# Optimization experiments

Hardware: AMD Instinct MI355X
Metric: run time of the kernel (lower is better)

## Reference

```python
import jax, jax.numpy as jnp
import numpy as np

N = 40000   # nodes
E = 600000  # edges
G = 64      # graphs
DIN = 128   # input feature dim
H = 128     # hidden_channels
L = 3       # num_layers


def setup_inputs() -> dict:
    key = jax.random.key(0)
    ks = jax.random.split(key, 16)
    s = 0.05
    inp = {}
    inp["x"] = jax.random.normal(ks[0], (N, DIN), jnp.float32)
    inp["edge_attr"] = jax.random.normal(ks[1], (E,), jnp.float32)
    inp["node_w"] = jax.random.normal(ks[2], (DIN, H), jnp.float32) * s
    inp["node_b"] = jnp.zeros((H,), jnp.float32)
    inp["edge_w"] = jax.random.normal(ks[3], (1, H), jnp.float32) * s
    inp["edge_b"] = jnp.zeros((H,), jnp.float32)
    inp["t"] = jnp.ones((L,), jnp.float32)  # learn_t init 1.0
    inp["lin1_w"] = jax.random.normal(ks[4], (L, H, 2 * H), jnp.float32) * s
    inp["lin1_b"] = jnp.zeros((L, 2 * H), jnp.float32)
    inp["ln1_g"] = jnp.ones((L, 2 * H), jnp.float32)
    inp["ln1_bt"] = jnp.zeros((L, 2 * H), jnp.float32)
    inp["lin2_w"] = jax.random.normal(ks[5], (L, 2 * H, H), jnp.float32) * s
    inp["lin2_b"] = jnp.zeros((L, H), jnp.float32)
    inp["blk_g"] = jnp.ones((L, H), jnp.float32)
    inp["blk_b"] = jnp.zeros((L, H), jnp.float32)
    inp["hw1"] = jax.random.normal(ks[6], (H, H // 2), jnp.float32) * s
    inp["hb1"] = jnp.zeros((H // 2,), jnp.float32)
    inp["hw2"] = jax.random.normal(ks[7], (H // 2, H // 4), jnp.float32) * s
    inp["hb2"] = jnp.zeros((H // 4,), jnp.float32)
    inp["hw3"] = jax.random.normal(ks[8], (H // 4, 1), jnp.float32) * s
    inp["hb3"] = jnp.zeros((1,), jnp.float32)
    inp["edge_index"] = jax.random.randint(ks[9], (2, E), 0, N, jnp.int32)
    inp["batch"] = jnp.sort(jax.random.randint(ks[10], (N,), 0, G, jnp.int32))
    return inp


def _layer_norm(v, g, b):
    mu = jnp.mean(v, axis=-1, keepdims=True)
    var = jnp.var(v, axis=-1, keepdims=True)
    return (v - mu) * jax.lax.rsqrt(var + 1e-5) * g + b


def reference(x, edge_attr, node_w, node_b, edge_w, edge_b, t,
              lin1_w, lin1_b, ln1_g, ln1_bt, lin2_w, lin2_b,
              blk_g, blk_b, hw1, hb1, hw2, hb2, hw3, hb3,
              edge_index, batch):
    src, dst = edge_index[0], edge_index[1]
    h = x @ node_w + node_b                       # [N, H]
    ea = edge_attr[:, None] @ edge_w + edge_b     # [E, H]

    def genconv(xn, i):
        # message: relu(x_j + e) + eps
        msg = jax.nn.relu(xn[src] + ea) + 1e-7    # [E, H]
        # scatter-softmax over dst with learnable temperature t
        logit = msg * t[i]
        m = jax.ops.segment_max(logit, dst, num_segments=N)
        m = jnp.where(jnp.isfinite(m), m, 0.0)    # isolated nodes
        ex = jnp.exp(logit - m[dst])
        den = jax.ops.segment_sum(ex, dst, num_segments=N)
        agg = jax.ops.segment_sum(ex * msg, dst, num_segments=N) / jnp.maximum(den, 1e-16)
        o = agg + xn                              # add root
        # GENConv MLP: Linear(H,2H) -> LayerNorm -> ReLU -> Linear(2H,H)
        o = jax.nn.relu(_layer_norm(o @ lin1_w[i] + lin1_b[i], ln1_g[i], ln1_bt[i]))
        return o @ lin2_w[i] + lin2_b[i]

    # layer 0: bare conv (as in the torch forward)
    h = genconv(h, 0)
    # layers 1..L-1: DeepGCNLayer res+ (norm -> act -> [dropout=id in eval] -> conv -> residual)
    for i in range(1, L):
        r = jax.nn.relu(_layer_norm(h, blk_g[i], blk_b[i]))
        h = h + genconv(r, i)
    # final norm+act uses layer 0's norm/act
    h = jax.nn.relu(_layer_norm(h, blk_g[0], blk_b[0]))
    # global mean pool over graphs
    cnt = jax.ops.segment_sum(jnp.ones((N,), h.dtype), batch, num_segments=G)
    pooled = jax.ops.segment_sum(h, batch, num_segments=G) / jnp.maximum(cnt, 1.0)[:, None]
    # MLP head (dropout = identity in eval)
    o = jax.nn.relu(pooled @ hw1 + hb1)
    o = jax.nn.relu(o @ hw2 + hb2)
    return o @ hw3 + hb3                          # [G, 1]
```

## Files before the change

### kernel.cpp

```cpp
#include <hip/hip_runtime.h>
#include <math.h>

#define NN 40000
#define NE 600000
#define NG 64
#define DIM_IN 128
#define HH 128
#define HH2 256

using half8 = __attribute__((ext_vector_type(8))) _Float16;
using half4 = __attribute__((ext_vector_type(4))) _Float16;
using h2    = __attribute__((ext_vector_type(2))) _Float16;
using f4    = __attribute__((ext_vector_type(4))) float;

__device__ __forceinline__ int lower_bound_dev(const int* a, int n, int key) {
    int lo = 0, hi = n;
    while (lo < hi) { int mid = (lo + hi) >> 1; if (a[mid] < key) lo = mid + 1; else hi = mid; }
    return lo;
}

#define NX (NN*DIM_IN)
#define NX4 (NX/4)
__global__ void convert_kernel(const float* __restrict__ x, const float* __restrict__ node_w,
                               const float* __restrict__ lin1_w, const float* __restrict__ lin2_w,
                               _Float16* __restrict__ xh, _Float16* __restrict__ nwt,
                               _Float16* __restrict__ w1t, _Float16* __restrict__ w2t)
{
    int id = blockIdx.x * blockDim.x + threadIdx.x;
    if (id < NX4) {
        float4 v = *(const float4*)(x + (size_t)id * 4);
        half4 o; o.x = (_Float16)v.x; o.y = (_Float16)v.y; o.z = (_Float16)v.z; o.w = (_Float16)v.w;
        *(half4*)(xh + (size_t)id * 4) = o;
        return;
    }
    id -= NX4;
    if (id < 16384) { int n = id >> 7, k = id & 127; nwt[id] = (_Float16)node_w[k*128 + n]; return; }
    id -= 16384;
    if (id < 98304) {
        int l = id >> 15, r = id & 32767;
        int n = r >> 7, k = r & 127;
        w1t[id] = (_Float16)lin1_w[l*32768 + k*256 + n];
        return;
    }
    id -= 98304;
    if (id < 98304) {
        int l = id >> 15, r = id & 32767;
        int n = r >> 8, k = r & 255;
        w2t[id] = (_Float16)lin2_w[l*32768 + k*128 + n];
    }
}

__global__ void count_rank_kernel(const int* __restrict__ dst, int* __restrict__ counts,
                                  int* __restrict__ rank) {
    int e = blockIdx.x * blockDim.x + threadIdx.x;
    if (e < NE) rank[e] = atomicAdd(&counts[dst[e]], 1);
}

__global__ __launch_bounds__(1024) void scanA_kernel(const int* __restrict__ counts,
                                                     int* __restrict__ tmp, int* __restrict__ btot) {
    __shared__ int wpre[16];
    int t = threadIdx.x, lane = t & 63, wid = t >> 6;
    int i = blockIdx.x * 1024 + t;
    int v = (i < NN) ? counts[i] : 0;
    int s = v;
    #pragma unroll
    for (int off = 1; off < 64; off <<= 1) {
        int u = __shfl_up(s, off, 64);
        if (lane >= off) s += u;
    }
    if (lane == 63) wpre[wid] = s;
    __syncthreads();
    if (t == 0) {
        int run = 0;
        #pragma unroll
        for (int j = 0; j < 16; ++j) { int xv = wpre[j]; wpre[j] = run; run += xv; }
        btot[blockIdx.x] = run;
    }
    __syncthreads();
    if (i < NN) tmp[i] = s + wpre[wid];
}

__global__ __launch_bounds__(64) void scanB_kernel(const int* __restrict__ btot,
                                                   int* __restrict__ boff, int nb) {
    int t = threadIdx.x;
    int v = (t < nb) ? btot[t] : 0;
    int s = v;
    #pragma unroll
    for (int off = 1; off < 64; off <<= 1) {
        int u = __shfl_up(s, off, 64);
        if (t >= off) s += u;
    }
    if (t < nb) boff[t] = s - v;
}

__global__ __launch_bounds__(1024) void scanC_kernel(const int* __restrict__ tmp,
                                                     const int* __restrict__ boff,
                                                     int* __restrict__ rowp) {
    int i = blockIdx.x * 1024 + threadIdx.x;
    if (i < NN) rowp[i + 1] = tmp[i] + boff[blockIdx.x];
    if (i == 0) rowp[0] = 0;
}

__global__ void fill2_kernel(const int* __restrict__ src, const int* __restrict__ dst,
                             const float* __restrict__ eattr, const int* __restrict__ rowp,
                             const int* __restrict__ rank, int2* __restrict__ rec) {
    int e = blockIdx.x * blockDim.x + threadIdx.x;
    if (e < NE) {
        int pos = rowp[dst[e]] + rank[e];
        rec[pos] = make_int2(src[e], __float_as_int(eattr[e]));
    }
}

__global__ __launch_bounds__(256) void agg_kernel(
    const _Float16* __restrict__ xh,
    const int* __restrict__ row_ptr,
    const int2* __restrict__ rec,
    const float* __restrict__ ew, const float* __restrict__ eb,
    const float* __restrict__ tptr, int layer,
    _Float16* __restrict__ oh)
{
    int d = blockIdx.x * 4 + (threadIdx.x >> 6);
    int lane = threadIdx.x & 63;
    int c0 = 2 * lane;
    float tc = tptr[layer];
    float ew0 = ew[c0], eb0 = eb[c0];
    float ew1 = ew[c0 + 1], eb1 = eb[c0 + 1];
    int beg = row_ptr[d], end = row_ptr[d + 1];
    float den0 = 0.f, num0 = 0.f, den1 = 0.f, num1 = 0.f;
    for (int base = beg; base < end; base += 64) {
        int cnt = min(64, end - base);
        int2 mv = rec[base + min(lane, cnt - 1)];
        int sv = mv.x;
        float av = __int_as_float(mv.y);
        h2 gA[8], gB[8]; float aA[8], aB[8];
        auto issue = [&](h2 (&g)[8], float (&aa)[8], int j0) {
            #pragma unroll
            for (int u = 0; u < 8; ++u) {
                int jj = min(j0 + u, cnt - 1);
                int s = __shfl(sv, jj, 64);
                aa[u] = __shfl(av, jj, 64);
                g[u] = *(const h2*)(xh + ((size_t)s << 7) + c0);
            }
        };
        auto consume = [&](h2 (&g)[8], float (&aa)[8], int j0) {
            int lim = min(8, cnt - j0);
            #pragma unroll
            for (int u = 0; u < 8; ++u) {
                if (u < lim) {
                    float m0 = fmaxf(__fmaf_rn(aa[u], ew0, eb0) + (float)g[u].x, 0.f) + 1e-7f;
                    float m1 = fmaxf(__fmaf_rn(aa[u], ew1, eb1) + (float)g[u].y, 0.f) + 1e-7f;
                    float e0 = __expf(m0 * tc), e1 = __expf(m1 * tc);
                    den0 += e0; num0 = __fmaf_rn(e0, m0, num0);
                    den1 += e1; num1 = __fmaf_rn(e1, m1, num1);
                }
            }
        };
        issue(gA, aA, 0);
        for (int j0 = 0; j0 < cnt; j0 += 16) {
            if (j0 + 8 < cnt)  issue(gB, aB, j0 + 8);
            consume(gA, aA, j0);
            if (j0 + 16 < cnt) issue(gA, aA, j0 + 16);
            if (j0 + 8 < cnt)  consume(gB, aB, j0 + 8);
        }
    }
    h2 sv2 = *(const h2*)(xh + ((size_t)d << 7) + c0);
    float o0 = num0 / fmaxf(den0, 1e-16f) + (float)sv2.x;
    float o1 = num1 / fmaxf(den1, 1e-16f) + (float)sv2.y;
    h2 ov; ov.x = (_Float16)o0; ov.y = (_Float16)o1;
    *(h2*)(oh + ((size_t)d << 7) + c0) = ov;
}

__global__ __launch_bounds__(256) void gemm_mfma(
    const _Float16* __restrict__ A, const _Float16* __restrict__ Bt,
    const float* __restrict__ bias, _Float16* __restrict__ C,
    int M, int N, int K)
{
    constexpr int LDA = 40;
    __shared__ _Float16 As[64 * LDA];
    __shared__ _Float16 Bs[128 * LDA];
    int t = threadIdx.x;
    int row0 = blockIdx.y * 64;
    int col0 = blockIdx.x * 128;
    int w = t >> 6, lane = t & 63;
    int wm = w & 1, wn = w >> 1;
    int q = lane >> 4, l16 = lane & 15;
    f4 acc[2][4];
    #pragma unroll
    for (int i = 0; i < 2; ++i)
        #pragma unroll
        for (int j = 0; j < 4; ++j)
            acc[i][j] = (f4){0.f, 0.f, 0.f, 0.f};

    for (int k0 = 0; k0 < K; k0 += 32) {
        {
            int r = t >> 2, seg = t & 3;
            *(float4*)&As[r * LDA + seg * 8] =
                *(const float4*)(A + (size_t)(row0 + r) * K + k0 + seg * 8);
        }
        #pragma unroll
        for (int i = 0; i < 2; ++i) {
            int idx = t + i * 256;
            int r = idx >> 2, seg = idx & 3;
            *(float4*)&Bs[r * LDA + seg * 8] =
                *(const float4*)(Bt + (size_t)(col0 + r) * K + k0 + seg * 8);
        }
        __syncthreads();
        half8 af[2], bf[4];
        #pragma unroll
        for (int i = 0; i < 2; ++i)
            af[i] = *(const half8*)&As[(wm * 32 + i * 16 + l16) * LDA + q * 8];
        #pragma unroll
        for (int j = 0; j < 4; ++j)
            bf[j] = *(const half8*)&Bs[(wn * 64 + j * 16 + l16) * LDA + q * 8];
        #pragma unroll
        for (int i = 0; i < 2; ++i)
            #pragma unroll
            for (int j = 0; j < 4; ++j)
                acc[i][j] = __builtin_amdgcn_mfma_f32_16x16x32_f16(af[i], bf[j], acc[i][j], 0, 0, 0);
        __syncthreads();
    }
    #pragma unroll
    for (int j = 0; j < 4; ++j) {
        int col = col0 + wn * 64 + j * 16 + l16;
        float bv = bias[col];
        #pragma unroll
        for (int i = 0; i < 2; ++i) {
            int rbase = row0 + wm * 32 + i * 16 + q * 4;
            #pragma unroll
            for (int rg = 0; rg < 4; ++rg)
                C[(size_t)(rbase + rg) * N + col] = (_Float16)(acc[i][j][rg] + bv);
        }
    }
}

template<int RES>
__global__ __launch_bounds__(256) void mlp_fused(
    const _Float16* __restrict__ Ain,
    const _Float16* __restrict__ w1t,
    const float* __restrict__ b1,
    const float* __restrict__ g1, const float* __restrict__ bt1,
    const _Float16* __restrict__ w2t,
    const float* __restrict__ b2,
    float* __restrict__ h,
    const float* __restrict__ bg, const float* __restrict__ bb,
    _Float16* __restrict__ xout)
{
    constexpr int LDA = 136;
    constexpr int LDB = 40;
    constexpr int LDM = 264;
    __shared__ _Float16 As[64 * LDA];
    __shared__ _Float16 Bs[256 * LDB];
    __shared__ _Float16 midh[64 * LDM];
    __shared__ float ssum[64][2], ssum2[64][2];
    int t = threadIdx.x;
    int row0 = blockIdx.x * 64;
    int w = t >> 6, lane = t & 63;
    int wm = w & 1, wn = w >> 1;
    int q = lane >> 4, l16 = lane & 15;

    #pragma unroll
    for (int p = 0; p < 4; ++p) {
        int idx = t + p * 256;
        int r = idx >> 4, seg = idx & 15;
        *(float4*)&As[r * LDA + seg * 8] =
            *(const float4*)(Ain + (size_t)(row0 + r) * 128 + seg * 8);
    }

    f4 acc[2][8];
    #pragma unroll
    for (int i = 0; i < 2; ++i)
        #pragma unroll
        for (int j = 0; j < 8; ++j)
            acc[i][j] = (f4){0.f, 0.f, 0.f, 0.f};
    for (int k0 = 0; k0 < 128; k0 += 32) {
        #pragma unroll
        for (int p = 0; p < 4; ++p) {
            int idx = t + p * 256;
            int r = idx >> 2, seg = idx & 3;
            *(float4*)&Bs[r * LDB + seg * 8] =
                *(const float4*)(w1t + (size_t)r * 128 + k0 + seg * 8);
        }
        __syncthreads();
        half8 af[2], bf[8];
        #pragma unroll
        for (int i = 0; i < 2; ++i)
            af[i] = *(const half8*)&As[(wm * 32 + i * 16 + l16) * LDA + k0 + q * 8];
        #pragma unroll
        for (int j = 0; j < 8; ++j)
            bf[j] = *(const half8*)&Bs[(wn * 128 + j * 16 + l16) * LDB + q * 8];
        #pragma unroll
        for (int i = 0; i < 2; ++i)
            #pragma unroll
            for (int j = 0; j < 8; ++j)
                acc[i][j] = __builtin_amdgcn_mfma_f32_16x16x32_f16(af[i], bf[j], acc[i][j], 0, 0, 0);
        __syncthreads();
    }

    float b1v[8], g1v[8], bt1v[8];
    #pragma unroll
    for (int j = 0; j < 8; ++j) {
        int col = wn * 128 + j * 16 + l16;
        b1v[j] = b1[col]; g1v[j] = g1[col]; bt1v[j] = bt1[col];
    }
    float vals[2][8][4];
    #pragma unroll
    for (int i = 0; i < 2; ++i)
        #pragma unroll
        for (int j = 0; j < 8; ++j)
            #pragma unroll
            for (int rg = 0; rg < 4; ++rg)
                vals[i][j][rg] = acc[i][j][rg] + b1v[j];
    #pragma unroll
    for (int i = 0; i < 2; ++i) {
        #pragma unroll
        for (int rg = 0; rg < 4; ++rg) {
            float ps = 0.f, ps2 = 0.f;
            #pragma unroll
            for (int j = 0; j < 8; ++j) { float v = vals[i][j][rg]; ps += v; ps2 += v * v; }
            #pragma unroll
            for (int off = 1; off < 16; off <<= 1) {
                ps  += __shfl_xor(ps,  off, 16);
                ps2 += __shfl_xor(ps2, off, 16);
            }
            if (l16 == 0) {
                int row = wm * 32 + i * 16 + q * 4 + rg;
                ssum[row][wn] = ps; ssum2[row][wn] = ps2;
            }
        }
    }
    __syncthreads();
    #pragma unroll
    for (int i = 0; i < 2; ++i) {
        #pragma unroll
        for (int rg = 0; rg < 4; ++rg) {
            int row = wm * 32 + i * 16 + q * 4 + rg;
            float S = ssum[row][0] + ssum[row][1];
            float S2 = ssum2[row][0] + ssum2[row][1];
            float mu = S * (1.0f / 256.0f);
            float var = S2 * (1.0f / 256.0f) - mu * mu;
            float rstd = rsqrtf(var + 1e-5f);
            #pragma unroll
            for (int j = 0; j < 8; ++j) {
                int col = wn * 128 + j * 16 + l16;
                float o = fmaxf((vals[i][j][rg] - mu) * rstd * g1v[j] + bt1v[j], 0.f);
                midh[row * LDM + col] = (_Float16)o;
            }
        }
    }
    __syncthreads();

    f4 acc2[2][4];
    #pragma unroll
    for (int i = 0; i < 2; ++i)
        #pragma unroll
        for (int j = 0; j < 4; ++j)
            acc2[i][j] = (f4){0.f, 0.f, 0.f, 0.f};
    for (int k0 = 0; k0 < 256; k0 += 32) {
        #pragma unroll
        for (int p = 0; p < 2; ++p) {
            int idx = t + p * 256;
            int r = idx >> 2, seg = idx & 3;
            *(float4*)&Bs[r * LDB + seg * 8] =
                *(const float4*)(w2t + (size_t)r * 256 + k0 + seg * 8);
        }
        __syncthreads();
        half8 af2[2], bf2[4];
        #pragma unroll
        for (int i = 0; i < 2; ++i)
            af2[i] = *(const half8*)&midh[(wm * 32 + i * 16 + l16) * LDM + k0 + q * 8];
        #pragma unroll
        for (int j = 0; j < 4; ++j)
            bf2[j] = *(const half8*)&Bs[(wn * 64 + j * 16 + l16) * LDB + q * 8];
        #pragma unroll
        for (int i = 0; i < 2; ++i)
            #pragma unroll
            for (int j = 0; j < 4; ++j)
                acc2[i][j] = __builtin_amdgcn_mfma_f32_16x16x32_f16(af2[i], bf2[j], acc2[i][j], 0, 0, 0);
        __syncthreads();
    }

    float b2v[4], bgv[4], bbv[4];
    #pragma unroll
    for (int j = 0; j < 4; ++j) {
        int col = wn * 64 + j * 16 + l16;
        b2v[j] = b2[col]; bgv[j] = bg[col]; bbv[j] = bb[col];
    }
    float ov[2][4][4];
    #pragma unroll
    for (int i = 0; i < 2; ++i) {
        #pragma unroll
        for (int rg = 0; rg < 4; ++rg) {
            int row = wm * 32 + i * 16 + q * 4 + rg;
            #pragma unroll
            for (int j = 0; j < 4; ++j) {
                int col = wn * 64 + j * 16 + l16;
                float v = acc2[i][j][rg] + b2v[j];
                size_t gidx = (size_t)(row0 + row) * 128 + col;
                if (RES) v += h[gidx];
                h[gidx] = v;
                ov[i][j][rg] = v;
            }
        }
    }
    #pragma unroll
    for (int i = 0; i < 2; ++i) {
        #pragma unroll
        for (int rg = 0; rg < 4; ++rg) {
            float ps = 0.f, ps2 = 0.f;
            #pragma unroll
            for (int j = 0; j < 4; ++j) { float v = ov[i][j][rg]; ps += v; ps2 += v * v; }
            #pragma unroll
            for (int off = 1; off < 16; off <<= 1) {
                ps  += __shfl_xor(ps,  off, 16);
                ps2 += __shfl_xor(ps2, off, 16);
            }
            if (l16 == 0) {
                int row = wm * 32 + i * 16 + q * 4 + rg;
                ssum[row][wn] = ps; ssum2[row][wn] = ps2;
            }
        }
    }
    __syncthreads();
    #pragma unroll
    for (int i = 0; i < 2; ++i) {
        #pragma unroll
        for (int rg = 0; rg < 4; ++rg) {
            int row = wm * 32 + i * 16 + q * 4 + rg;
            float S = ssum[row][0] + ssum[row][1];
            float S2 = ssum2[row][0] + ssum2[row][1];
            float mu = S * (1.0f / 128.0f);
            float var = S2 * (1.0f / 128.0f) - mu * mu;
            float rstd = rsqrtf(var + 1e-5f);
            #pragma unroll
            for (int j = 0; j < 4; ++j) {
                int col = wn * 64 + j * 16 + l16;
                float o = fmaxf((ov[i][j][rg] - mu) * rstd * bgv[j] + bbv[j], 0.f);
                xout[(size_t)(row0 + row) * 128 + col] = (_Float16)o;
            }
        }
    }
}

__global__ __launch_bounds__(128) void pool_kernel(
    const _Float16* __restrict__ f, const int* __restrict__ batch, float* __restrict__ pooled)
{
    int g = blockIdx.x;
    int chunk = blockIdx.y;
    int c = threadIdx.x;
    int s = lower_bound_dev(batch, NN, g);
    int e = lower_bound_dev(batch, NN, g + 1);
    int len = e - s;
    if (len <= 0) return;
    int nch = gridDim.y;
    int per = (len + nch - 1) / nch;
    int cs = s + chunk * per;
    int ce = min(cs + per, e);
    if (cs >= ce) return;
    float acc = 0.f;
    for (int n = cs; n < ce; ++n) acc += (float)f[(size_t)n * HH + c];
    atomicAdd(&pooled[g * HH + c], acc);
}

__global__ __launch_bounds__(128) void head_kernel(
    const float* __restrict__ pooled, const int* __restrict__ batch,
    const float* __restrict__ hw1, const float* __restrict__ hb1,
    const float* __restrict__ hw2, const float* __restrict__ hb2,
    const float* __restrict__ hw3, const float* __restrict__ hb3,
    float* __restrict__ out)
{
    __shared__ float p[HH];
    __shared__ float o1[64];
    __shared__ float o2[32];
    int g = blockIdx.x;
    int t = threadIdx.x;
    int s = lower_bound_dev(batch, NN, g);
    int e = lower_bound_dev(batch, NN, g + 1);
    float cnt = fmaxf((float)(e - s), 1.0f);
    p[t] = pooled[g * HH + t] / cnt;
    __syncthreads();
    if (t < 64) {
        float acc = hb1[t];
        for (int k = 0; k < HH; ++k) acc += p[k] * hw1[k * 64 + t];
        o1[t] = fmaxf(acc, 0.f);
    }
    __syncthreads();
    if (t < 32) {
        float acc = hb2[t];
        for (int k = 0; k < 64; ++k) acc += o1[k] * hw2[k * 32 + t];
        o2[t] = fmaxf(acc, 0.f);
    }
    __syncthreads();
    if (t == 0) {
        float acc = hb3[0];
        for (int k = 0; k < 32; ++k) acc += o2[k] * hw3[k];
        out[g] = acc;
    }
}

extern "C" void kernel_launch(void* const* d_in, const int* in_sizes, int n_in,
                              void* d_out, int out_size, void* d_ws, size_t ws_size,
                              hipStream_t stream)
{
    const float* x      = (const float*)d_in[0];
    const float* eattr  = (const float*)d_in[1];
    const float* node_w = (const float*)d_in[2];
    const float* node_b = (const float*)d_in[3];
    const float* edge_w = (const float*)d_in[4];
    const float* edge_b = (const float*)d_in[5];
    const float* tptr   = (const float*)d_in[6];
    const float* lin1_w = (const float*)d_in[7];
    const float* lin1_b = (const float*)d_in[8];
    const float* ln1_g  = (const float*)d_in[9];
    const float* ln1_bt = (const float*)d_in[10];
    const float* lin2_w = (const float*)d_in[11];
    const float* lin2_b = (const float*)d_in[12];
    const float* blk_g  = (const float*)d_in[13];
    const float* blk_b  = (const float*)d_in[14];
    const float* hw1    = (const float*)d_in[15];
    const float* hb1    = (const float*)d_in[16];
    const float* hw2    = (const float*)d_in[17];
    const float* hb2    = (const float*)d_in[18];
    const float* hw3    = (const float*)d_in[19];
    const float* hb3    = (const float*)d_in[20];
    const int*   eidx   = (const int*)d_in[21];
    const int*   batch  = (const int*)d_in[22];
    const int* src = eidx;
    const int* dst = eidx + NE;
    float* out = (float*)d_out;

    char* ws = (char*)d_ws;
    size_t off = 0;
    auto carve = [&](size_t bytes) -> char* {
        char* p = ws + off;
        off = (off + bytes + 255) & ~(size_t)255;
        return p;
    };
    float*    h      = (float*)carve((size_t)NN * HH * 4);
    _Float16* xh_in  = (_Float16*)carve((size_t)NX * 2);
    _Float16* xnh    = (_Float16*)carve((size_t)NN * HH * 2);
    _Float16* oh     = (_Float16*)carve((size_t)NN * HH * 2);
    _Float16* rh     = (_Float16*)carve((size_t)NN * HH * 2);
    _Float16* nwt    = (_Float16*)carve((size_t)16384 * 2);
    _Float16* w1t    = (_Float16*)carve((size_t)98304 * 2);
    _Float16* w2t    = (_Float16*)carve((size_t)98304 * 2);
    int*      counts = (int*)carve((size_t)NN * 4);
    int*      rank   = (int*)carve((size_t)NE * 4);
    int*      tmp    = (int*)carve((size_t)NN * 4);
    int*      btot   = (int*)carve((size_t)64 * 4);
    int*      boff   = (int*)carve((size_t)64 * 4);
    int*      rowp   = (int*)carve((size_t)(NN + 1) * 4);
    int2*     rec    = (int2*)carve((size_t)NE * 8);
    float*    pooled = (float*)carve((size_t)NG * HH * 4);

    hipMemsetAsync(counts, 0, (size_t)NN * 4, stream);
    hipMemsetAsync(pooled, 0, (size_t)NG * HH * 4, stream);

    {
        int total = NX4 + 16384 + 98304 + 98304;
        convert_kernel<<<(total + 255) / 256, 256, 0, stream>>>(
            x, node_w, lin1_w, lin2_w, xh_in, nwt, w1t, w2t);
    }
    const int NB = (NN + 1023) / 1024;
    count_rank_kernel<<<(NE + 255) / 256, 256, 0, stream>>>(dst, counts, rank);
    scanA_kernel<<<NB, 1024, 0, stream>>>(counts, tmp, btot);
    scanB_kernel<<<1, 64, 0, stream>>>(btot, boff, NB);
    scanC_kernel<<<NB, 1024, 0, stream>>>(tmp, boff, rowp);
    fill2_kernel<<<(NE + 255) / 256, 256, 0, stream>>>(src, dst, eattr, rowp, rank, rec);

    gemm_mfma<<<dim3(1, NN / 64), 256, 0, stream>>>(xh_in, nwt, node_b, xnh, NN, HH, DIM_IN);

    agg_kernel<<<NN / 4, 256, 0, stream>>>(xnh, rowp, rec, edge_w, edge_b, tptr, 0, oh);
    mlp_fused<0><<<NN / 64, 256, 0, stream>>>(
        oh, w1t, lin1_b, ln1_g, ln1_bt, w2t, lin2_b,
        h, blk_g + 1 * HH, blk_b + 1 * HH, xnh);
    agg_kernel<<<NN / 4, 256, 0, stream>>>(xnh, rowp, rec, edge_w, edge_b, tptr, 1, oh);
    mlp_fused<1><<<NN / 64, 256, 0, stream>>>(
        oh, w1t + 32768, lin1_b + HH2, ln1_g + HH2, ln1_bt + HH2, w2t + 32768, lin2_b + HH,
        h, blk_g + 2 * HH, blk_b + 2 * HH, xnh);
    agg_kernel<<<NN / 4, 256, 0, stream>>>(xnh, rowp, rec, edge_w, edge_b, tptr, 2, oh);
    mlp_fused<1><<<NN / 64, 256, 0, stream>>>(
        oh, w1t + 2 * 32768, lin1_b + 2 * HH2, ln1_g + 2 * HH2, ln1_bt + 2 * HH2,
        w2t + 2 * 32768, lin2_b + 2 * HH,
        h, blk_g, blk_b, rh);

    pool_kernel<<<dim3(NG, 8), 128, 0, stream>>>(rh, batch, pooled);
    head_kernel<<<NG, 128, 0, stream>>>(pooled, batch, hw1, hb1, hw2, hb2, hw3, hb3, out);
}
```

Measured before the change: 394.0 us.

## Fuse setup kernels, read MLP weights directly from global, shrink shared memory

Folds the edge count/rank pass and the pooled-buffer zeroing into the conversion kernel. Merges the two-level scan's middle step into scanC through a per-block reduction of block totals. In mlp_fused, weights are read straight from global/L2 instead of being staged through shared memory. The As and mid buffers now share one shared-memory region with an XOR swizzle, and launch bounds request higher occupancy. Ping-pong feature buffers are added so the in-place overwrite is avoided. The risk is more global weight traffic per wave and the cost of the correctness barriers that shared buffer reuse requires.

```diff
diff --git a/kernel.cpp b/kernel.cpp
--- a/kernel.cpp
+++ b/kernel.cpp
@@ -23,6 +23,8 @@
 #define NX4 (NX/4)
 __global__ void convert_kernel(const float* __restrict__ x, const float* __restrict__ node_w,
                                const float* __restrict__ lin1_w, const float* __restrict__ lin2_w,
+                               const int* __restrict__ dst, int* __restrict__ counts,
+                               int* __restrict__ rank, float* __restrict__ pooled,
                                _Float16* __restrict__ xh, _Float16* __restrict__ nwt,
                                _Float16* __restrict__ w1t, _Float16* __restrict__ w2t)
 {
@@ -47,13 +49,12 @@
         int l = id >> 15, r = id & 32767;
         int n = r >> 8, k = r & 255;
         w2t[id] = (_Float16)lin2_w[l*32768 + k*128 + n];
-    }
-}
-
-__global__ void count_rank_kernel(const int* __restrict__ dst, int* __restrict__ counts,
-                                  int* __restrict__ rank) {
-    int e = blockIdx.x * blockDim.x + threadIdx.x;
-    if (e < NE) rank[e] = atomicAdd(&counts[dst[e]], 1);
+        return;
+    }
+    id -= 98304;
+    if (id < NG * HH) { pooled[id] = 0.f; return; }
+    id -= NG * HH;
+    if (id < NE) rank[id] = atomicAdd(&counts[dst[id]], 1);
 }
 
 __global__ __launch_bounds__(1024) void scanA_kernel(const int* __restrict__ counts,
@@ -80,24 +81,20 @@
     if (i < NN) tmp[i] = s + wpre[wid];
 }
 
-__global__ __launch_bounds__(64) void scanB_kernel(const int* __restrict__ btot,
-                                                   int* __restrict__ boff, int nb) {
+__global__ __launch_bounds__(1024) void scanC_kernel(const int* __restrict__ tmp,
+                                                     const int* __restrict__ btot,
+                                                     int* __restrict__ rowp) {
+    __shared__ int s_off;
     int t = threadIdx.x;
-    int v = (t < nb) ? btot[t] : 0;
-    int s = v;
-    #pragma unroll
-    for (int off = 1; off < 64; off <<= 1) {
-        int u = __shfl_up(s, off, 64);
-        if (t >= off) s += u;
-    }
-    if (t < nb) boff[t] = s - v;
-}
-
-__global__ __launch_bounds__(1024) void scanC_kernel(const int* __restrict__ tmp,
-                                                     const int* __restrict__ boff,
-                                                     int* __restrict__ rowp) {
-    int i = blockIdx.x * 1024 + threadIdx.x;
-    if (i < NN) rowp[i + 1] = tmp[i] + boff[blockIdx.x];
+    if (t < 64) {
+        int v = (t < blockIdx.x) ? btot[t] : 0;
+        #pragma unroll
+        for (int o = 32; o > 0; o >>= 1) v += __shfl_down(v, o, 64);
+        if (t == 0) s_off = v;
+    }
+    __syncthreads();
+    int i = blockIdx.x * 1024 + t;
+    if (i < NN) rowp[i + 1] = tmp[i] + s_off;
     if (i == 0) rowp[0] = 0;
 }
 
@@ -234,24 +231,21 @@
 }
 
 template<int RES>
-__global__ __launch_bounds__(256) void mlp_fused(
+__global__ __launch_bounds__(256, 4) void mlp_fused(
     const _Float16* __restrict__ Ain,
-    const _Float16* __restrict__ w1t,
-    const float* __restrict__ b1,
+    const _Float16* __restrict__ w1t, const float* __restrict__ b1,
     const float* __restrict__ g1, const float* __restrict__ bt1,
-    const _Float16* __restrict__ w2t,
-    const float* __restrict__ b2,
+    const _Float16* __restrict__ w2t, const float* __restrict__ b2,
     float* __restrict__ h,
     const float* __restrict__ bg, const float* __restrict__ bb,
     _Float16* __restrict__ xout)
 {
     constexpr int LDA = 136;
-    constexpr int LDB = 40;
-    constexpr int LDM = 264;
-    __shared__ _Float16 As[64 * LDA];
-    __shared__ _Float16 Bs[256 * LDB];
-    __shared__ _Float16 midh[64 * LDM];
-    __shared__ float ssum[64][2], ssum2[64][2];
+    __shared__ __align__(16) char smem[33792];
+    _Float16* As   = (_Float16*)smem;
+    _Float16* midh = (_Float16*)smem;
+    float* ssum    = (float*)(smem + 32768);
+    float* ssum2   = (float*)(smem + 33280);
     int t = threadIdx.x;
     int row0 = blockIdx.x * 64;
     int w = t >> 6, lane = t & 63;
@@ -265,6 +259,7 @@
         *(float4*)&As[r * LDA + seg * 8] =
             *(const float4*)(Ain + (size_t)(row0 + r) * 128 + seg * 8);
     }
+    __syncthreads();
 
     f4 acc[2][8];
     #pragma unroll
@@ -272,28 +267,20 @@
         #pragma unroll
         for (int j = 0; j < 8; ++j)
             acc[i][j] = (f4){0.f, 0.f, 0.f, 0.f};
+    #pragma unroll
     for (int k0 = 0; k0 < 128; k0 += 32) {
-        #pragma unroll
-        for (int p = 0; p < 4; ++p) {
-            int idx = t + p * 256;
-            int r = idx >> 2, seg = idx & 3;
-            *(float4*)&Bs[r * LDB + seg * 8] =
-                *(const float4*)(w1t + (size_t)r * 128 + k0 + seg * 8);
-        }
-        __syncthreads();
         half8 af[2], bf[8];
         #pragma unroll
         for (int i = 0; i < 2; ++i)
             af[i] = *(const half8*)&As[(wm * 32 + i * 16 + l16) * LDA + k0 + q * 8];
         #pragma unroll
         for (int j = 0; j < 8; ++j)
-            bf[j] = *(const half8*)&Bs[(wn * 128 + j * 16 + l16) * LDB + q * 8];
+            bf[j] = *(const half8*)(w1t + (size_t)(wn * 128 + j * 16 + l16) * 128 + k0 + q * 8);
         #pragma unroll
         for (int i = 0; i < 2; ++i)
             #pragma unroll
             for (int j = 0; j < 8; ++j)
                 acc[i][j] = __builtin_amdgcn_mfma_f32_16x16x32_f16(af[i], bf[j], acc[i][j], 0, 0, 0);
-        __syncthreads();
     }
 
     float b1v[8], g1v[8], bt1v[8];
@@ -324,7 +311,7 @@
             }
             if (l16 == 0) {
                 int row = wm * 32 + i * 16 + q * 4 + rg;
-                ssum[row][wn] = ps; ssum2[row][wn] = ps2;
+                ssum[row * 2 + wn] = ps; ssum2[row * 2 + wn] = ps2;
             }
         }
     }
@@ -334,8 +321,8 @@
         #pragma unroll
         for (int rg = 0; rg < 4; ++rg) {
             int row = wm * 32 + i * 16 + q * 4 + rg;
-            float S = ssum[row][0] + ssum[row][1];
-            float S2 = ssum2[row][0] + ssum2[row][1];
+            float S = ssum[row * 2 + 0] + ssum[row * 2 + 1];
+            float S2 = ssum2[row * 2 + 0] + ssum2[row * 2 + 1];
             float mu = S * (1.0f / 256.0f);
             float var = S2 * (1.0f / 256.0f) - mu * mu;
             float rstd = rsqrtf(var + 1e-5f);
@@ -343,7 +330,8 @@
             for (int j = 0; j < 8; ++j) {
                 int col = wn * 128 + j * 16 + l16;
                 float o = fmaxf((vals[i][j][rg] - mu) * rstd * g1v[j] + bt1v[j], 0.f);
-                midh[row * LDM + col] = (_Float16)o;
+                int pg = (col >> 3) ^ (row & 31);
+                midh[row * 256 + (pg << 3) + (col & 7)] = (_Float16)o;
             }
         }
     }
@@ -355,28 +343,23 @@
         #pragma unroll
         for (int j = 0; j < 4; ++j)
             acc2[i][j] = (f4){0.f, 0.f, 0.f, 0.f};
+    #pragma unroll
     for (int k0 = 0; k0 < 256; k0 += 32) {
-        #pragma unroll
-        for (int p = 0; p < 2; ++p) {
-            int idx = t + p * 256;
-            int r = idx >> 2, seg = idx & 3;
-            *(float4*)&Bs[r * LDB + seg * 8] =
-                *(const float4*)(w2t + (size_t)r * 256 + k0 + seg * 8);
-        }
-        __syncthreads();
         half8 af2[2], bf2[4];
         #pragma unroll
-        for (int i = 0; i < 2; ++i)
-            af2[i] = *(const half8*)&midh[(wm * 32 + i * 16 + l16) * LDM + k0 + q * 8];
+        for (int i = 0; i < 2; ++i) {
+            int rr = wm * 32 + i * 16 + l16;
+            int pg = ((k0 >> 3) + q) ^ (rr & 31);
+            af2[i] = *(const half8*)&midh[rr * 256 + (pg << 3)];
+        }
         #pragma unroll
         for (int j = 0; j < 4; ++j)
-            bf2[j] = *(const half8*)&Bs[(wn * 64 + j * 16 + l16) * LDB + q * 8];
+            bf2[j] = *(const half8*)(w2t + (size_t)(wn * 64 + j * 16 + l16) * 256 + k0 + q * 8);
         #pragma unroll
         for (int i = 0; i < 2; ++i)
             #pragma unroll
             for (int j = 0; j < 4; ++j)
                 acc2[i][j] = __builtin_amdgcn_mfma_f32_16x16x32_f16(af2[i], bf2[j], acc2[i][j], 0, 0, 0);
-        __syncthreads();
     }
 
     float b2v[4], bgv[4], bbv[4];
@@ -402,6 +385,7 @@
             }
         }
     }
+    __syncthreads();
     #pragma unroll
     for (int i = 0; i < 2; ++i) {
         #pragma unroll
@@ -416,7 +400,7 @@
             }
             if (l16 == 0) {
                 int row = wm * 32 + i * 16 + q * 4 + rg;
-                ssum[row][wn] = ps; ssum2[row][wn] = ps2;
+                ssum[row * 2 + wn] = ps; ssum2[row * 2 + wn] = ps2;
             }
         }
     }
@@ -426,8 +410,8 @@
         #pragma unroll
         for (int rg = 0; rg < 4; ++rg) {
             int row = wm * 32 + i * 16 + q * 4 + rg;
-            float S = ssum[row][0] + ssum[row][1];
-            float S2 = ssum2[row][0] + ssum2[row][1];
+            float S = ssum[row * 2 + 0] + ssum[row * 2 + 1];
+            float S2 = ssum2[row * 2 + 0] + ssum2[row * 2 + 1];
             float mu = S * (1.0f / 128.0f);
             float var = S2 * (1.0f / 128.0f) - mu * mu;
             float rstd = rsqrtf(var + 1e-5f);
@@ -537,7 +521,8 @@
     };
     float*    h      = (float*)carve((size_t)NN * HH * 4);
     _Float16* xh_in  = (_Float16*)carve((size_t)NX * 2);
-    _Float16* xnh    = (_Float16*)carve((size_t)NN * HH * 2);
+    _Float16* xa     = (_Float16*)carve((size_t)NN * HH * 2);
+    _Float16* xb     = (_Float16*)carve((size_t)NN * HH * 2);
     _Float16* oh     = (_Float16*)carve((size_t)NN * HH * 2);
     _Float16* rh     = (_Float16*)carve((size_t)NN * HH * 2);
     _Float16* nwt    = (_Float16*)carve((size_t)16384 * 2);
@@ -547,37 +532,33 @@
     int*      rank   = (int*)carve((size_t)NE * 4);
     int*      tmp    = (int*)carve((size_t)NN * 4);
     int*      btot   = (int*)carve((size_t)64 * 4);
-    int*      boff   = (int*)carve((size_t)64 * 4);
     int*      rowp   = (int*)carve((size_t)(NN + 1) * 4);
     int2*     rec    = (int2*)carve((size_t)NE * 8);
     float*    pooled = (float*)carve((size_t)NG * HH * 4);
 
     hipMemsetAsync(counts, 0, (size_t)NN * 4, stream);
-    hipMemsetAsync(pooled, 0, (size_t)NG * HH * 4, stream);
 
     {
-        int total = NX4 + 16384 + 98304 + 98304;
+        int total = NX4 + 16384 + 98304 + 98304 + NG * HH + NE;
         convert_kernel<<<(total + 255) / 256, 256, 0, stream>>>(
-            x, node_w, lin1_w, lin2_w, xh_in, nwt, w1t, w2t);
+            x, node_w, lin1_w, lin2_w, dst, counts, rank, pooled, xh_in, nwt, w1t, w2t);
     }
     const int NB = (NN + 1023) / 1024;
-    count_rank_kernel<<<(NE + 255) / 256, 256, 0, stream>>>(dst, counts, rank);
     scanA_kernel<<<NB, 1024, 0, stream>>>(counts, tmp, btot);
-    scanB_kernel<<<1, 64, 0, stream>>>(btot, boff, NB);
-    scanC_kernel<<<NB, 1024, 0, stream>>>(tmp, boff, rowp);
+    scanC_kernel<<<NB, 1024, 0, stream>>>(tmp, btot, rowp);
     fill2_kernel<<<(NE + 255) / 256, 256, 0, stream>>>(src, dst, eattr, rowp, rank, rec);
 
-    gemm_mfma<<<dim3(1, NN / 64), 256, 0, stream>>>(xh_in, nwt, node_b, xnh, NN, HH, DIM_IN);
-
-    agg_kernel<<<NN / 4, 256, 0, stream>>>(xnh, rowp, rec, edge_w, edge_b, tptr, 0, oh);
+    gemm_mfma<<<dim3(1, NN / 64), 256, 0, stream>>>(xh_in, nwt, node_b, xa, NN, HH, DIM_IN);
+
+    agg_kernel<<<NN / 4, 256, 0, stream>>>(xa, rowp, rec, edge_w, edge_b, tptr, 0, oh);
     mlp_fused<0><<<NN / 64, 256, 0, stream>>>(
         oh, w1t, lin1_b, ln1_g, ln1_bt, w2t, lin2_b,
-        h, blk_g + 1 * HH, blk_b + 1 * HH, xnh);
-    agg_kernel<<<NN / 4, 256, 0, stream>>>(xnh, rowp, rec, edge_w, edge_b, tptr, 1, oh);
+        h, blk_g + 1 * HH, blk_b + 1 * HH, xb);
+    agg_kernel<<<NN / 4, 256, 0, stream>>>(xb, rowp, rec, edge_w, edge_b, tptr, 1, oh);
     mlp_fused<1><<<NN / 64, 256, 0, stream>>>(
         oh, w1t + 32768, lin1_b + HH2, ln1_g + HH2, ln1_bt + HH2, w2t + 32768, lin2_b + HH,
-        h, blk_g + 2 * HH, blk_b + 2 * HH, xnh);
-    agg_kernel<<<NN / 4, 256, 0, stream>>>(xnh, rowp, rec, edge_w, edge_b, tptr, 2, oh);
+        h, blk_g + 2 * HH, blk_b + 2 * HH, xa);
+    agg_kernel<<<NN / 4, 256, 0, stream>>>(xa, rowp, rec, edge_w, edge_b, tptr, 2, oh);
     mlp_fused<1><<<NN / 64, 256, 0, stream>>>(
         oh, w1t + 2 * 32768, lin1_b + 2 * HH2, ln1_g + 2 * HH2, ln1_bt + 2 * HH2,
         w2t + 2 * 32768, lin2_b + 2 * HH,
```

Measured after the change: 404.8 us. 2.7% more time.
